# Kernel optimization log

Measured on AMD Instinct MI355X. Metric: run time of the kernel, lower is better.

Reference implementation:

```python
import jax, jax.numpy as jnp
import numpy as np

N = 8192        # nodes
E = 262144      # edges (avg degree 32)
D = 128         # input_dim
H = 128         # hidden_dim
O = 64          # output_dim (classes)
C = 4096        # codebook_size
LAMB_EDGE = 1.0
LAMB_NODE = 1.0
COMMIT_W = 0.25


def l2norm(x):
    return x / jnp.clip(jnp.linalg.norm(x, axis=-1, keepdims=True), 1e-12)


def graph_conv(x, W, b, src, dst, n):
    # DGL GraphConv, norm='both': D_out^{-1/2} on src, sum-aggregate, D_in^{-1/2} on dst, then xW+b, relu
    ones = jnp.ones(src.shape[0], x.dtype)
    deg_out = jax.ops.segment_sum(ones, src, num_segments=n)
    deg_in = jax.ops.segment_sum(ones, dst, num_segments=n)
    norm_src = jnp.where(deg_out > 0, jax.lax.rsqrt(jnp.maximum(deg_out, 1e-12)), 0.0)
    norm_dst = jnp.where(deg_in > 0, jax.lax.rsqrt(jnp.maximum(deg_in, 1e-12)), 0.0)
    h = x * norm_src[:, None]
    m = jax.ops.segment_sum(h[src], dst, num_segments=n)  # message passing (irregular gather/scatter)
    h = m * norm_dst[:, None]
    return jax.nn.relu(h @ W + b)


def setup_inputs() -> dict:
    key = jax.random.key(0)
    ks = jax.random.split(key, 16)
    feats = jax.random.normal(ks[0], (N, D), jnp.float32)
    src = jax.random.randint(ks[1], (E,), 0, N)
    dst = jax.random.randint(ks[2], (E,), 0, N)
    s = 1.0 / np.sqrt(D)
    sh = 1.0 / np.sqrt(H)
    return {
        'feats': feats, 'src': src, 'dst': dst,
        'W1': jax.random.normal(ks[3], (D, D), jnp.float32) * s,
        'b1': jnp.zeros((D,), jnp.float32),
        'W2': jax.random.normal(ks[4], (D, H), jnp.float32) * s,
        'b2': jnp.zeros((H,), jnp.float32),
        'dec1_W': jax.random.normal(ks[5], (D, D), jnp.float32) * s,
        'dec1_b': jnp.zeros((D,), jnp.float32),
        'dec2_W': jax.random.normal(ks[6], (D, D), jnp.float32) * s,
        'dec2_b': jnp.zeros((D,), jnp.float32),
        'lin_W': jax.random.normal(ks[7], (H, O), jnp.float32) * sh,
        'lin_b': jnp.zeros((O,), jnp.float32),
        'codebook': jax.random.normal(ks[8], (C, D), jnp.float32),
    }


def reference(feats, src, dst, W1, b1, W2, b2, dec1_W, dec1_b, dec2_W, dec2_b, lin_W, lin_b, codebook):
    n = feats.shape[0]
    # layer 1: GraphConv(D -> D)
    h1 = graph_conv(feats, W1, b1, src, dst, n)  # [N, D]

    # VectorQuantize with cosine similarity codebook
    xn = l2norm(h1)
    cn = l2norm(codebook)                 # [C, D]
    dist = xn @ cn.T                      # [N, C] cosine similarity
    ind = jnp.argmax(dist, axis=-1)       # [N]
    q = cn[ind]                           # [N, D] nearest (normalized) codes
    commit_loss = COMMIT_W * jnp.mean((jax.lax.stop_gradient(q) - h1) ** 2)
    quantized = h1 + jax.lax.stop_gradient(q - h1)  # straight-through

    quantized_edge = quantized @ dec1_W + dec1_b
    quantized_node = quantized @ dec2_W + dec2_b
    feature_rec_loss = LAMB_NODE * jnp.mean((h1 - quantized_node) ** 2)

    # dense adjacency reconstruction
    adj = jnp.zeros((n, n), feats.dtype).at[src, dst].set(1.0)
    adj_q = quantized_edge @ quantized_edge.T          # [N, N]
    adj_q = (adj_q - adj_q.min()) / (adj_q.max() - adj_q.min())
    edge_rec_loss = LAMB_EDGE * jnp.sqrt(jnp.mean((adj - adj_q) ** 2))

    # layer 2: GraphConv(D -> H) on quantized_edge, then linear head
    h3 = graph_conv(quantized_edge, W2, b2, src, dst, n)
    out = h3 @ lin_W + lin_b                           # [N, O]

    loss = feature_rec_loss + edge_rec_loss + commit_loss
    h_list = (h1, quantized, h3)
    return (h_list, out, loss, dist, cn)
```

## Files before the change

### kernel.cpp

```cpp
#include <hip/hip_runtime.h>
#include <cstdint>

constexpr int N = 8192, E = 262144, D = 128, O = 64, C = 4096;

#define DEV __device__ __forceinline__

typedef short s8v __attribute__((ext_vector_type(8)));
typedef float f4v __attribute__((ext_vector_type(4)));

DEV unsigned fmap(float f) {
  unsigned u = __float_as_uint(f);
  return (u & 0x80000000u) ? ~u : (u | 0x80000000u);
}
DEV unsigned short f2bf(float f) {
  uint32_t b = __float_as_uint(f);
  return (unsigned short)((b + 0x7FFFu + ((b >> 16) & 1u)) >> 16);
}


__global__ __launch_bounds__(256) void k_degree(const int* __restrict__ src, const int* __restrict__ dst,
    uint32_t* __restrict__ bits, int* __restrict__ dego, int* __restrict__ degi,
    uint32_t* __restrict__ scal_u) {
  int e = blockIdx.x * 256 + threadIdx.x;
  int s = src[e], d = dst[e];
  atomicAdd(&dego[s], 1);
  atomicAdd(&degi[d], 1);
  unsigned idx = (unsigned)s * 8192u + (unsigned)d;
  unsigned bit = 1u << (idx & 31);
  unsigned old = atomicOr(&bits[idx >> 5], bit);
  bool isnew = !(old & bit);
  unsigned long long b = __ballot(isnew);
  if ((threadIdx.x & 63) == 0) atomicAdd(&scal_u[2], (unsigned)__popcll(b));
}

__global__ __launch_bounds__(256) void k_norms(const int* __restrict__ dego, const int* __restrict__ degi,
                                               float* __restrict__ nsrc, float* __restrict__ ndst) {
  int i = blockIdx.x * 256 + threadIdx.x;
  if (i >= N) return;
  int a = dego[i], b = degi[i];
  nsrc[i] = a > 0 ? 1.0f / sqrtf((float)a) : 0.0f;
  ndst[i] = b > 0 ? 1.0f / sqrtf((float)b) : 0.0f;
}

__global__ __launch_bounds__(1024) void k_scan(const int* __restrict__ degi, int* __restrict__ rowptr,
                                               int* __restrict__ cursor) {
  __shared__ int sh[1024];
  int tid = threadIdx.x;
  int base = tid * 8;
  int v[8];
  int s = 0;
#pragma unroll
  for (int j = 0; j < 8; ++j) { v[j] = degi[base + j]; s += v[j]; }
  sh[tid] = s;
  __syncthreads();
  for (int off = 1; off < 1024; off <<= 1) {
    int t = (tid >= off) ? sh[tid - off] : 0;
    __syncthreads();
    sh[tid] += t;
    __syncthreads();
  }
  int run = (tid == 0) ? 0 : sh[tid - 1];
#pragma unroll
  for (int j = 0; j < 8; ++j) { rowptr[base + j] = run; cursor[base + j] = run; run += v[j]; }
  if (tid == 1023) rowptr[N] = run;
}

__global__ __launch_bounds__(256) void k_scatter(const int* __restrict__ src, const int* __restrict__ dst,
                                                 int* __restrict__ cursor, int* __restrict__ csr) {
  int e = blockIdx.x * 256 + threadIdx.x;
  int d = dst[e];
  int pos = atomicAdd(&cursor[d], 1);
  csr[pos] = src[e];
}

__global__ __launch_bounds__(256) void k_scale(const float4* __restrict__ in, const float* __restrict__ norm,
                                               float4* __restrict__ out) {
  int i = blockIdx.x * 256 + threadIdx.x;
  if (i >= N * 32) return;
  float s = norm[i >> 5];
  float4 v = in[i];
  v.x *= s; v.y *= s; v.z *= s; v.w *= s;
  out[i] = v;
}

__global__ __launch_bounds__(256) void k_tobf16(const float4* __restrict__ in, ushort4* __restrict__ out) {
  int i = blockIdx.x * 256 + threadIdx.x;
  if (i >= N * 32) return;
  float4 v = in[i];
  ushort4 o;
  o.x = f2bf(v.x); o.y = f2bf(v.y); o.z = f2bf(v.z); o.w = f2bf(v.w);
  out[i] = o;
}

__global__ __launch_bounds__(128) void k_aggregate(const int* __restrict__ rowptr, const int* __restrict__ csr,
    const float* __restrict__ tmp, const float* __restrict__ ndst, float* __restrict__ out) {
  int row = blockIdx.x, t = threadIdx.x;
  int e0 = rowptr[row], e1 = rowptr[row + 1];
  float acc = 0.f;
  int e = e0;
  for (; e + 4 <= e1; e += 4) {
    int s0 = csr[e], s1 = csr[e + 1], s2 = csr[e + 2], s3 = csr[e + 3];
    acc += tmp[s0 * 128 + t];
    acc += tmp[s1 * 128 + t];
    acc += tmp[s2 * 128 + t];
    acc += tmp[s3 * 128 + t];
  }
  for (; e < e1; ++e) acc += tmp[csr[e] * 128 + t];
  out[row * 128 + t] = acc * ndst[row];
}

__global__ __launch_bounds__(256) void k_l2norm(const float* __restrict__ in, float* __restrict__ out_al,
                                                float* __restrict__ out_extra, int rows) {
  int wave = threadIdx.x >> 6, lane = threadIdx.x & 63;
  int row = blockIdx.x * 4 + wave;
  if (row >= rows) return;
  float2 v = ((const float2*)in)[row * 64 + lane];
  float ss = v.x * v.x + v.y * v.y;
#pragma unroll
  for (int o = 32; o > 0; o >>= 1) ss += __shfl_xor(ss, o);
  float den = fmaxf(sqrtf(ss), 1e-12f);
  float ox = v.x / den, oy = v.y / den;
  ((float2*)out_al)[row * 64 + lane] = make_float2(ox, oy);
  if (out_extra != nullptr) {
    out_extra[row * 128 + 2 * lane] = ox;
    out_extra[row * 128 + 2 * lane + 1] = oy;
  }
}

template <int CO, bool RELU>
__global__ __launch_bounds__(256, 2) void k_mm(const float* __restrict__ A, const float* __restrict__ W,
    const float* __restrict__ bias, float* __restrict__ out) {
  constexpr int CG = CO / 4;
  constexpr int RG = 256 / CG;
  constexpr int TR = RG * 4;
  constexpr int WIT = (64 * CG) / 256;
  __shared__ __align__(16) float Al[TR * 128];
  __shared__ __align__(16) float Wl[64 * CO];
  int tid = threadIdx.x;
  int cg = tid % CG, rg = tid / CG;
  int rbase = blockIdx.x * TR;
#pragma unroll
  for (int it = 0; it < TR / 8; ++it) {
    int idx = tid + it * 256;
    int r = idx >> 5, c = idx & 31;
    *(float4*)&Al[r * 128 + c * 4] = *(const float4*)&A[(rbase + r) * 128 + c * 4];
  }
  float acc[4][4] = {};
  for (int kc = 0; kc < 128; kc += 64) {
    __syncthreads();
#pragma unroll
    for (int it = 0; it < WIT; ++it) {
      int idx = tid + it * 256;
      int r = idx / CG, c = idx % CG;
      *(float4*)&Wl[r * CO + c * 4] = *(const float4*)&W[(kc + r) * CO + c * 4];
    }
    __syncthreads();
#pragma unroll
    for (int k = 0; k < 64; ++k) {
      float4 w4 = *(const float4*)&Wl[k * CO + cg * 4];
#pragma unroll
      for (int i = 0; i < 4; ++i) {
        float a = Al[(rg * 4 + i) * 128 + kc + k];
        acc[i][0] += a * w4.x; acc[i][1] += a * w4.y; acc[i][2] += a * w4.z; acc[i][3] += a * w4.w;
      }
    }
  }
  float4 b4 = *(const float4*)&bias[cg * 4];
#pragma unroll
  for (int i = 0; i < 4; ++i) {
    float4 o;
    o.x = acc[i][0] + b4.x; o.y = acc[i][1] + b4.y; o.z = acc[i][2] + b4.z; o.w = acc[i][3] + b4.w;
    if (RELU) { o.x = fmaxf(o.x, 0.f); o.y = fmaxf(o.y, 0.f); o.z = fmaxf(o.z, 0.f); o.w = fmaxf(o.w, 0.f); }
    *(float4*)&out[(rbase + rg * 4 + i) * CO + cg * 4] = o;
  }
}

__global__ __launch_bounds__(256) void k_gemm(const float* __restrict__ A, const float* __restrict__ B,
    float* __restrict__ dout, unsigned long long* __restrict__ amax) {
  int bx = blockIdx.x, by = blockIdx.y;
  int rbase = by * 128, cbase = bx * 128;
  __shared__ __align__(16) float Al[128 * 36];
  __shared__ __align__(16) float Bl[128 * 36];
  int tid = threadIdx.x;
  int tx = tid & 15, ty = tid >> 4;
  float acc[8][8];
#pragma unroll
  for (int i = 0; i < 8; ++i)
#pragma unroll
    for (int j = 0; j < 8; ++j) acc[i][j] = 0.f;

  for (int kc = 0; kc < 128; kc += 32) {
#pragma unroll
    for (int it = 0; it < 4; ++it) {
      int idx = tid + it * 256;
      int r = idx >> 3, c = idx & 7;
      *(float4*)&Al[r * 36 + c * 4] = *(const float4*)&A[(rbase + r) * 128 + kc + c * 4];
      *(float4*)&Bl[r * 36 + c * 4] = *(const float4*)&B[(cbase + r) * 128 + kc + c * 4];
    }
    __syncthreads();
#pragma unroll 1
    for (int k4 = 0; k4 < 8; ++k4) {
      float4 a[8];
#pragma unroll
      for (int i = 0; i < 8; ++i) a[i] = *(const float4*)&Al[(ty + (i << 4)) * 36 + (k4 << 2)];
#pragma unroll
      for (int j = 0; j < 8; ++j) {
        float4 b = *(const float4*)&Bl[(tx + (j << 4)) * 36 + (k4 << 2)];
#pragma unroll
        for (int i = 0; i < 8; ++i)
          acc[i][j] += a[i].x * b.x + a[i].y * b.y + a[i].z * b.z + a[i].w * b.w;
      }
    }
    __syncthreads();
  }

  float bestv[8];
  int bestc[8];
#pragma unroll
  for (int i = 0; i < 8; ++i) { bestv[i] = -3.4e38f; bestc[i] = 0; }
#pragma unroll
  for (int i = 0; i < 8; ++i) {
    int row = rbase + ty + (i << 4);
#pragma unroll
    for (int j = 0; j < 8; ++j) {
      int col = cbase + tx + (j << 4);
      float v = acc[i][j];
      dout[row * 4096 + col] = v;
      if (v > bestv[i]) { bestv[i] = v; bestc[i] = col; }
    }
  }
  unsigned long long* sc = (unsigned long long*)Al;
#pragma unroll
  for (int i = 0; i < 8; ++i)
    sc[(ty + (i << 4)) * 16 + tx] =
        (((unsigned long long)fmap(bestv[i])) << 32) | (unsigned long long)(0xFFFFFFFFu - (unsigned)bestc[i]);
  __syncthreads();
  if (tid < 128) {
    unsigned long long m = 0ull;
#pragma unroll
    for (int k = 0; k < 16; ++k) {
      unsigned long long t = sc[tid * 16 + k];
      m = t > m ? t : m;
    }
    atomicMax(&amax[rbase + tid], m);
  }
}

__global__ __launch_bounds__(256) void k_adjq(const unsigned short* __restrict__ qb,
    const uint32_t* __restrict__ bits,
    double* __restrict__ p_sum, double* __restrict__ p_sq, double* __restrict__ p_es,
    float* __restrict__ p_mn, float* __restrict__ p_mx) {
  int bx = blockIdx.x, by = blockIdx.y;
  int pid = by * gridDim.x + bx;
  int tid = threadIdx.x;
  if (bx < by) {
    if (tid == 0) {
      p_sum[pid] = 0.0; p_sq[pid] = 0.0; p_es[pid] = 0.0;
      p_mn[pid] = 3.4e38f; p_mx[pid] = -3.4e38f;
    }
    return;
  }
  int rbase = by * 128, cbase = bx * 128;
  __shared__ unsigned short Ab[128 * 132];
  __shared__ unsigned short Bb[128 * 132];
#pragma unroll
  for (int it = 0; it < 8; ++it) {
    int idx = tid + it * 256;
    int r = idx >> 4, ch = idx & 15;
    *(s8v*)&Ab[r * 132 + ch * 8] = *(const s8v*)&qb[(rbase + r) * 128 + ch * 8];
    *(s8v*)&Bb[r * 132 + ch * 8] = *(const s8v*)&qb[(cbase + r) * 128 + ch * 8];
  }
  __syncthreads();
  int wave = tid >> 6, lane = tid & 63;
  int l15 = lane & 15, quad = lane >> 4;
  int wr = wave * 32;
  f4v acc[2][8];
#pragma unroll
  for (int rt = 0; rt < 2; ++rt)
#pragma unroll
    for (int ct = 0; ct < 8; ++ct) acc[rt][ct] = {0.f, 0.f, 0.f, 0.f};
  s8v a[2][4];
#pragma unroll
  for (int rt = 0; rt < 2; ++rt)
#pragma unroll
    for (int kq = 0; kq < 4; ++kq)
      a[rt][kq] = *(const s8v*)&Ab[(wr + rt * 16 + l15) * 132 + kq * 32 + quad * 8];
#pragma unroll
  for (int ct = 0; ct < 8; ++ct) {
    s8v b[4];
#pragma unroll
    for (int kq = 0; kq < 4; ++kq)
      b[kq] = *(const s8v*)&Bb[(ct * 16 + l15) * 132 + kq * 32 + quad * 8];
#pragma unroll
    for (int rt = 0; rt < 2; ++rt)
#pragma unroll
      for (int kq = 0; kq < 4; ++kq)
        acc[rt][ct] = __builtin_amdgcn_mfma_f32_16x16x32_bf16(a[rt][kq], b[kq], acc[rt][ct], 0, 0, 0);
  }
  __syncthreads();
  uint32_t* bl = (uint32_t*)Ab;
  uint32_t* blT = bl + 512;
#pragma unroll
  for (int it = 0; it < 2; ++it) {
    int idx = tid + it * 256;
    int r = idx >> 2, wq = idx & 3;
    bl[idx] = bits[(rbase + r) * 256 + (cbase >> 5) + wq];
    blT[idx] = bits[(cbase + r) * 256 + (rbase >> 5) + wq];
  }
  __syncthreads();
  float lsum = 0.f, lsq = 0.f, les = 0.f;
  float lmin = 3.4e38f, lmax = -3.4e38f;
  bool diag = (bx == by);
#pragma unroll
  for (int rt = 0; rt < 2; ++rt)
#pragma unroll
    for (int ct = 0; ct < 8; ++ct)
#pragma unroll
      for (int reg = 0; reg < 4; ++reg) {
        int lr = wr + rt * 16 + quad * 4 + reg;
        int lc = ct * 16 + l15;
        if (diag && lc < lr) continue;
        float v = acc[rt][ct][reg];
        bool ondiag = diag && (lc == lr);
        float wgt = ondiag ? 1.f : 2.f;
        lsum += wgt * v;
        lsq += wgt * v * v;
        lmin = fminf(lmin, v);
        lmax = fmaxf(lmax, v);
        unsigned eb = (bl[lr * 4 + (lc >> 5)] >> (lc & 31)) & 1u;
        if (!ondiag) eb += (blT[lc * 4 + (lr >> 5)] >> (lr & 31)) & 1u;
        if (eb) les += (float)eb * v;
      }
  double dsum = (double)lsum, dsq = (double)lsq, des = (double)les;
#pragma unroll
  for (int o = 32; o > 0; o >>= 1) {
    dsum += __shfl_xor(dsum, o);
    dsq += __shfl_xor(dsq, o);
    des += __shfl_xor(des, o);
    lmin = fminf(lmin, __shfl_xor(lmin, o));
    lmax = fmaxf(lmax, __shfl_xor(lmax, o));
  }
  double* shd = (double*)Bb;
  float* shf = (float*)(shd + 12);
  if (lane == 0) {
    shd[wave * 3 + 0] = dsum; shd[wave * 3 + 1] = dsq; shd[wave * 3 + 2] = des;
    shf[wave * 2 + 0] = lmin; shf[wave * 2 + 1] = lmax;
  }
  __syncthreads();
  if (tid == 0) {
    double s = 0.0, q = 0.0, e = 0.0;
    float m0 = 3.4e38f, m1 = -3.4e38f;
#pragma unroll
    for (int w0 = 0; w0 < 4; ++w0) {
      s += shd[w0 * 3 + 0]; q += shd[w0 * 3 + 1]; e += shd[w0 * 3 + 2];
      m0 = fminf(m0, shf[w0 * 2 + 0]); m1 = fmaxf(m1, shf[w0 * 2 + 1]);
    }
    p_sum[pid] = s; p_sq[pid] = q; p_es[pid] = e;
    p_mn[pid] = m0; p_mx[pid] = m1;
  }
}

__global__ __launch_bounds__(128) void k_q(const unsigned long long* __restrict__ amax,
    const float* __restrict__ cnws, const float* __restrict__ h1, float* __restrict__ qout,
    float* __restrict__ pq) {
  int row = blockIdx.x, t = threadIdx.x;
  unsigned long long key = amax[row];
  int col = (int)(0xFFFFFFFFu - (uint32_t)(key & 0xFFFFFFFFull));
  float q = cnws[col * 128 + t];
  qout[row * 128 + t] = q;
  float dd = q - h1[row * 128 + t];
  float ss = dd * dd;
#pragma unroll
  for (int o = 32; o > 0; o >>= 1) ss += __shfl_xor(ss, o);
  __shared__ float p[2];
  if ((t & 63) == 0) p[t >> 6] = ss;
  __syncthreads();
  if (t == 0) pq[row] = p[0] + p[1];
}

__global__ __launch_bounds__(256) void k_sqdiff(const float4* __restrict__ a, const float4* __restrict__ b,
                                                float* __restrict__ ps) {
  int i = blockIdx.x * 256 + threadIdx.x;
  float s = 0.f;
  const int total = N * 32;
  for (; i < total; i += gridDim.x * 256) {
    float4 x = a[i], y = b[i];
    float d0 = x.x - y.x, d1 = x.y - y.y, d2 = x.z - y.z, d3 = x.w - y.w;
    s += d0 * d0 + d1 * d1 + d2 * d2 + d3 * d3;
  }
#pragma unroll
  for (int o = 32; o > 0; o >>= 1) s += __shfl_xor(s, o);
  __shared__ float p[4];
  if ((threadIdx.x & 63) == 0) p[threadIdx.x >> 6] = s;
  __syncthreads();
  if (threadIdx.x == 0) ps[blockIdx.x] = p[0] + p[1] + p[2] + p[3];
}

__global__ __launch_bounds__(1024) void k_finish(const double* __restrict__ p_sum,
    const double* __restrict__ p_sq, const double* __restrict__ p_es,
    const float* __restrict__ p_mn, const float* __restrict__ p_mx,
    const float* __restrict__ pq, const float* __restrict__ ps,
    const uint32_t* __restrict__ scal_u, float* __restrict__ o_loss) {
  int tid = threadIdx.x;
  double sum = 0.0, sq = 0.0, es = 0.0, commit = 0.0, frec = 0.0;
  float mn = 3.4e38f, mx = -3.4e38f;
  for (int i = tid; i < 4096; i += 1024) {
    sum += p_sum[i]; sq += p_sq[i]; es += p_es[i];
    mn = fminf(mn, p_mn[i]); mx = fmaxf(mx, p_mx[i]);
  }
  for (int i = tid; i < 8192; i += 1024) commit += (double)pq[i];
  if (tid < 512) frec = (double)ps[tid];
#pragma unroll
  for (int o = 32; o > 0; o >>= 1) {
    sum += __shfl_xor(sum, o); sq += __shfl_xor(sq, o); es += __shfl_xor(es, o);
    commit += __shfl_xor(commit, o); frec += __shfl_xor(frec, o);
    mn = fminf(mn, __shfl_xor(mn, o)); mx = fmaxf(mx, __shfl_xor(mx, o));
  }
  __shared__ double shd[16][5];
  __shared__ float shf[16][2];
  int wave = tid >> 6, lane = tid & 63;
  if (lane == 0) {
    shd[wave][0] = sum; shd[wave][1] = sq; shd[wave][2] = es;
    shd[wave][3] = commit; shd[wave][4] = frec;
    shf[wave][0] = mn; shf[wave][1] = mx;
  }
  __syncthreads();
  if (tid == 0) {
    double s = 0, q = 0, e = 0, c = 0, f = 0;
    float m0 = 3.4e38f, m1 = -3.4e38f;
    for (int w0 = 0; w0 < 16; ++w0) {
      s += shd[w0][0]; q += shd[w0][1]; e += shd[w0][2]; c += shd[w0][3]; f += shd[w0][4];
      m0 = fminf(m0, shf[w0][0]); m1 = fmaxf(m1, shf[w0][1]);
    }
    double mnd = (double)m0, mxd = (double)m1, U = (double)scal_u[2];
    const double N2 = 67108864.0;
    double scl = 1.0 / (mxd - mnd);
    double mean = (scl * scl * (q - 2.0 * mnd * s + mnd * mnd * N2) - 2.0 * scl * (e - mnd * U) + U) / N2;
    *o_loss = (float)(f / 1048576.0 + sqrt(mean) + 0.25 * c / 1048576.0);
  }
}

extern "C" void kernel_launch(void* const* d_in, const int* in_sizes, int n_in,
                              void* d_out, int out_size, void* d_ws, size_t ws_size,
                              hipStream_t stream) {
  (void)in_sizes; (void)n_in; (void)out_size;
  const float* feats = (const float*)d_in[0];
  const int* src = (const int*)d_in[1];
  const int* dst = (const int*)d_in[2];
  const float* W1 = (const float*)d_in[3];
  const float* b1 = (const float*)d_in[4];
  const float* W2 = (const float*)d_in[5];
  const float* b2 = (const float*)d_in[6];
  const float* dec1W = (const float*)d_in[7];
  const float* dec1b = (const float*)d_in[8];
  const float* dec2W = (const float*)d_in[9];
  const float* dec2b = (const float*)d_in[10];
  const float* linW = (const float*)d_in[11];
  const float* linb = (const float*)d_in[12];
  const float* codebook = (const float*)d_in[13];

  float* out = (float*)d_out;
  float* o_h1 = out;
  float* o_q = out + 1048576;
  float* o_h3 = out + 2097152;
  float* o_out = out + 3145728;
  float* o_loss = out + 3670016;
  float* o_dist = out + 3670017;
  float* o_cn = out + 37224449;

  char* w = (char*)d_ws;
  size_t off = 0;
  auto alloc = [&](size_t b) { char* p = w + off; off = (off + b + 255) & ~(size_t)255; return p; };
  uint32_t* bits = (uint32_t*)alloc(8388608);
  int* dego = (int*)alloc(N * 4);
  int* degi = (int*)alloc(N * 4);
  unsigned long long* amax = (unsigned long long*)alloc(N * 8);
  uint32_t* scal_u = (uint32_t*)alloc(256);
  size_t zero_bytes = off;
  int* rowptr = (int*)alloc((N + 1) * 4);
  int* cursor = (int*)alloc(N * 4);
  int* csr = (int*)alloc(E * 4);
  float* nsrc = (float*)alloc(N * 4);
  float* ndst = (float*)alloc(N * 4);
  float* tmp = (float*)alloc((size_t)N * D * 4);
  float* agg = (float*)alloc((size_t)N * D * 4);
  float* xn = (float*)alloc((size_t)N * D * 4);
  float* cnws = (float*)alloc((size_t)C * D * 4);
  float* qe = (float*)alloc((size_t)N * D * 4);
  float* qn = (float*)alloc((size_t)N * D * 4);
  double* p_sum = (double*)alloc(4096 * 8);
  double* p_sq = (double*)alloc(4096 * 8);
  double* p_es = (double*)alloc(4096 * 8);
  float* p_mn = (float*)alloc(4096 * 4);
  float* p_mx = (float*)alloc(4096 * 4);
  float* pq = (float*)alloc(8192 * 4);
  float* ps = (float*)alloc(512 * 4);
  unsigned short* qb = (unsigned short*)tmp;
  if (ws_size < off) return;

  hipMemsetAsync(d_ws, 0, zero_bytes, stream);

  k_degree<<<E / 256, 256, 0, stream>>>(src, dst, bits, dego, degi, scal_u);
  k_norms<<<N / 256, 256, 0, stream>>>(dego, degi, nsrc, ndst);
  k_scan<<<1, 1024, 0, stream>>>(degi, rowptr, cursor);
  k_scatter<<<E / 256, 256, 0, stream>>>(src, dst, cursor, csr);

  k_scale<<<N * 32 / 256, 256, 0, stream>>>((const float4*)feats, nsrc, (float4*)tmp);
  k_aggregate<<<N, 128, 0, stream>>>(rowptr, csr, tmp, ndst, agg);
  k_mm<128, true><<<N / 32, 256, 0, stream>>>(agg, W1, b1, o_h1);

  k_l2norm<<<C / 4, 256, 0, stream>>>(codebook, cnws, o_cn, C);
  k_l2norm<<<N / 4, 256, 0, stream>>>(o_h1, xn, nullptr, N);
  k_gemm<<<dim3(C / 128, N / 128), 256, 0, stream>>>(xn, cnws, o_dist, amax);
  k_q<<<N, 128, 0, stream>>>(amax, cnws, o_h1, o_q, pq);

  k_mm<128, false><<<N / 32, 256, 0, stream>>>(o_q, dec1W, dec1b, qe);
  k_mm<128, false><<<N / 32, 256, 0, stream>>>(o_q, dec2W, dec2b, qn);
  k_sqdiff<<<512, 256, 0, stream>>>((const float4*)o_h1, (const float4*)qn, ps);

  k_tobf16<<<N * 32 / 256, 256, 0, stream>>>((const float4*)qe, (ushort4*)qb);
  k_adjq<<<dim3(N / 128, N / 128), 256, 0, stream>>>(qb, bits, p_sum, p_sq, p_es, p_mn, p_mx);

  k_scale<<<N * 32 / 256, 256, 0, stream>>>((const float4*)qe, nsrc, (float4*)tmp);
  k_aggregate<<<N, 128, 0, stream>>>(rowptr, csr, tmp, ndst, agg);
  k_mm<128, true><<<N / 32, 256, 0, stream>>>(agg, W2, b2, o_h3);
  k_mm<64, false><<<N / 64, 256, 0, stream>>>(o_h3, linW, linb, o_out);

  k_finish<<<1, 1024, 0, stream>>>(p_sum, p_sq, p_es, p_mn, p_mx, pq, ps, scal_u, o_loss);
}
```

Measured before the change: 544.1 us.

## Compute cosine-similarity GEMM with split-bf16 MFMA and exact fp32 argmax fallback

Replaces the fp32 FMA-based N×C cosine-similarity GEMM with an MFMA kernel that splits each operand into bf16 hi and lo parts and sums three products (hi·hi, lo·hi, hi·lo) to approximate fp32 accuracy. Each tile also records its top-2 values, and the quantize kernel reduces these per row. When the top-2 gap is below a threshold, it recomputes the argmax exactly in fp32 to keep index selection robust. The goal is to move the dominant 8192×4096×128 GEMM onto matrix cores, at the cost of two split kernels, extra partial buffers, and possible precision drift in the stored dist output.

After: 606.4 us. +11.5%, slower.

```diff
diff --git a/kernel.cpp b/kernel.cpp
--- a/kernel.cpp
+++ b/kernel.cpp
@@ -12,10 +12,15 @@
   unsigned u = __float_as_uint(f);
   return (u & 0x80000000u) ? ~u : (u | 0x80000000u);
 }
+DEV float funmap(unsigned u) {
+  unsigned o = (u & 0x80000000u) ? (u & 0x7FFFFFFFu) : ~u;
+  return __uint_as_float(o);
+}
 DEV unsigned short f2bf(float f) {
   uint32_t b = __float_as_uint(f);
   return (unsigned short)((b + 0x7FFFu + ((b >> 16) & 1u)) >> 16);
 }
+DEV float bf2f(unsigned short h) { return __uint_as_float((uint32_t)h << 16); }
 
 
 __global__ __launch_bounds__(256) void k_degree(const int* __restrict__ src, const int* __restrict__ dst,
@@ -92,6 +97,18 @@
   out[i] = o;
 }
 
+__global__ __launch_bounds__(256) void k_split(const float4* __restrict__ in,
+    ushort4* __restrict__ hi, ushort4* __restrict__ lo, int n4) {
+  int i = blockIdx.x * 256 + threadIdx.x;
+  if (i >= n4) return;
+  float4 v = in[i];
+  ushort4 h, l;
+  h.x = f2bf(v.x); h.y = f2bf(v.y); h.z = f2bf(v.z); h.w = f2bf(v.w);
+  l.x = f2bf(v.x - bf2f(h.x)); l.y = f2bf(v.y - bf2f(h.y));
+  l.z = f2bf(v.z - bf2f(h.z)); l.w = f2bf(v.w - bf2f(h.w));
+  hi[i] = h; lo[i] = l;
+}
+
 __global__ __launch_bounds__(128) void k_aggregate(const int* __restrict__ rowptr, const int* __restrict__ csr,
     const float* __restrict__ tmp, const float* __restrict__ ndst, float* __restrict__ out) {
   int row = blockIdx.x, t = threadIdx.x;
@@ -175,75 +192,196 @@
   }
 }
 
-__global__ __launch_bounds__(256) void k_gemm(const float* __restrict__ A, const float* __restrict__ B,
-    float* __restrict__ dout, unsigned long long* __restrict__ amax) {
+__global__ __launch_bounds__(256) void k_dist(
+    const unsigned short* __restrict__ xhi, const unsigned short* __restrict__ xlo,
+    const unsigned short* __restrict__ chi, const unsigned short* __restrict__ clo,
+    float* __restrict__ dout, unsigned long long* __restrict__ pbk, float* __restrict__ pbv2) {
   int bx = blockIdx.x, by = blockIdx.y;
   int rbase = by * 128, cbase = bx * 128;
-  __shared__ __align__(16) float Al[128 * 36];
-  __shared__ __align__(16) float Bl[128 * 36];
+  __shared__ __align__(16) unsigned short As[128 * 132];
+  __shared__ __align__(16) unsigned short Bs[128 * 132];
   int tid = threadIdx.x;
-  int tx = tid & 15, ty = tid >> 4;
-  float acc[8][8];
-#pragma unroll
-  for (int i = 0; i < 8; ++i)
-#pragma unroll
-    for (int j = 0; j < 8; ++j) acc[i][j] = 0.f;
-
-  for (int kc = 0; kc < 128; kc += 32) {
-#pragma unroll
-    for (int it = 0; it < 4; ++it) {
-      int idx = tid + it * 256;
-      int r = idx >> 3, c = idx & 7;
-      *(float4*)&Al[r * 36 + c * 4] = *(const float4*)&A[(rbase + r) * 128 + kc + c * 4];
-      *(float4*)&Bl[r * 36 + c * 4] = *(const float4*)&B[(cbase + r) * 128 + kc + c * 4];
-    }
-    __syncthreads();
-#pragma unroll 1
-    for (int k4 = 0; k4 < 8; ++k4) {
-      float4 a[8];
-#pragma unroll
-      for (int i = 0; i < 8; ++i) a[i] = *(const float4*)&Al[(ty + (i << 4)) * 36 + (k4 << 2)];
-#pragma unroll
-      for (int j = 0; j < 8; ++j) {
-        float4 b = *(const float4*)&Bl[(tx + (j << 4)) * 36 + (k4 << 2)];
-#pragma unroll
-        for (int i = 0; i < 8; ++i)
-          acc[i][j] += a[i].x * b.x + a[i].y * b.y + a[i].z * b.z + a[i].w * b.w;
+  int wave = tid >> 6, lane = tid & 63;
+  int l15 = lane & 15, quad = lane >> 4;
+  int wr = wave * 32;
+
+#pragma unroll
+  for (int it = 0; it < 8; ++it) {
+    int idx = tid + it * 256;
+    int r = idx >> 4, ch = idx & 15;
+    *(s8v*)&As[r * 132 + ch * 8] = *(const s8v*)&xhi[(rbase + r) * 128 + ch * 8];
+    *(s8v*)&Bs[r * 132 + ch * 8] = *(const s8v*)&chi[(cbase + r) * 128 + ch * 8];
+  }
+  __syncthreads();
+  s8v ah[2][4], al[2][4];
+#pragma unroll
+  for (int rt = 0; rt < 2; ++rt)
+#pragma unroll
+    for (int kq = 0; kq < 4; ++kq)
+      ah[rt][kq] = *(const s8v*)&As[(wr + rt * 16 + l15) * 132 + kq * 32 + quad * 8];
+  __syncthreads();
+#pragma unroll
+  for (int it = 0; it < 8; ++it) {
+    int idx = tid + it * 256;
+    int r = idx >> 4, ch = idx & 15;
+    *(s8v*)&As[r * 132 + ch * 8] = *(const s8v*)&xlo[(rbase + r) * 128 + ch * 8];
+  }
+  __syncthreads();
+#pragma unroll
+  for (int rt = 0; rt < 2; ++rt)
+#pragma unroll
+    for (int kq = 0; kq < 4; ++kq)
+      al[rt][kq] = *(const s8v*)&As[(wr + rt * 16 + l15) * 132 + kq * 32 + quad * 8];
+
+  f4v acc[2][8];
+#pragma unroll
+  for (int rt = 0; rt < 2; ++rt)
+#pragma unroll
+    for (int ct = 0; ct < 8; ++ct) acc[rt][ct] = {0.f, 0.f, 0.f, 0.f};
+
+#pragma unroll
+  for (int ct = 0; ct < 8; ++ct) {
+    s8v b[4];
+#pragma unroll
+    for (int kq = 0; kq < 4; ++kq)
+      b[kq] = *(const s8v*)&Bs[(ct * 16 + l15) * 132 + kq * 32 + quad * 8];
+#pragma unroll
+    for (int rt = 0; rt < 2; ++rt)
+#pragma unroll
+      for (int kq = 0; kq < 4; ++kq) {
+        acc[rt][ct] = __builtin_amdgcn_mfma_f32_16x16x32_bf16(ah[rt][kq], b[kq], acc[rt][ct], 0, 0, 0);
+        acc[rt][ct] = __builtin_amdgcn_mfma_f32_16x16x32_bf16(al[rt][kq], b[kq], acc[rt][ct], 0, 0, 0);
       }
-    }
-    __syncthreads();
-  }
-
-  float bestv[8];
-  int bestc[8];
-#pragma unroll
-  for (int i = 0; i < 8; ++i) { bestv[i] = -3.4e38f; bestc[i] = 0; }
-#pragma unroll
-  for (int i = 0; i < 8; ++i) {
-    int row = rbase + ty + (i << 4);
-#pragma unroll
-    for (int j = 0; j < 8; ++j) {
-      int col = cbase + tx + (j << 4);
-      float v = acc[i][j];
-      dout[row * 4096 + col] = v;
-      if (v > bestv[i]) { bestv[i] = v; bestc[i] = col; }
-    }
-  }
-  unsigned long long* sc = (unsigned long long*)Al;
-#pragma unroll
-  for (int i = 0; i < 8; ++i)
-    sc[(ty + (i << 4)) * 16 + tx] =
-        (((unsigned long long)fmap(bestv[i])) << 32) | (unsigned long long)(0xFFFFFFFFu - (unsigned)bestc[i]);
+  }
+  __syncthreads();
+#pragma unroll
+  for (int it = 0; it < 8; ++it) {
+    int idx = tid + it * 256;
+    int r = idx >> 4, ch = idx & 15;
+    *(s8v*)&Bs[r * 132 + ch * 8] = *(const s8v*)&clo[(cbase + r) * 128 + ch * 8];
+  }
+  __syncthreads();
+#pragma unroll
+  for (int ct = 0; ct < 8; ++ct) {
+    s8v b[4];
+#pragma unroll
+    for (int kq = 0; kq < 4; ++kq)
+      b[kq] = *(const s8v*)&Bs[(ct * 16 + l15) * 132 + kq * 32 + quad * 8];
+#pragma unroll
+    for (int rt = 0; rt < 2; ++rt)
+#pragma unroll
+      for (int kq = 0; kq < 4; ++kq)
+        acc[rt][ct] = __builtin_amdgcn_mfma_f32_16x16x32_bf16(ah[rt][kq], b[kq], acc[rt][ct], 0, 0, 0);
+  }
+
+  float b1v[2][4], b2v[2][4];
+  unsigned c1v[2][4];
+#pragma unroll
+  for (int rt = 0; rt < 2; ++rt)
+#pragma unroll
+    for (int reg = 0; reg < 4; ++reg) { b1v[rt][reg] = -3.4e38f; b2v[rt][reg] = -3.4e38f; c1v[rt][reg] = 0; }
+#pragma unroll
+  for (int rt = 0; rt < 2; ++rt)
+#pragma unroll
+    for (int ct = 0; ct < 8; ++ct)
+#pragma unroll
+      for (int reg = 0; reg < 4; ++reg) {
+        float v = acc[rt][ct][reg];
+        int row = rbase + wr + rt * 16 + quad * 4 + reg;
+        int col = cbase + ct * 16 + l15;
+        dout[(size_t)row * 4096 + col] = v;
+        if (v > b1v[rt][reg]) { b2v[rt][reg] = b1v[rt][reg]; b1v[rt][reg] = v; c1v[rt][reg] = (unsigned)col; }
+        else if (v > b2v[rt][reg]) b2v[rt][reg] = v;
+      }
+  __syncthreads();
+  unsigned long long* sck = (unsigned long long*)As;
+  float* scv = (float*)Bs;
+#pragma unroll
+  for (int rt = 0; rt < 2; ++rt)
+#pragma unroll
+    for (int reg = 0; reg < 4; ++reg) {
+      int rloc = wr + rt * 16 + quad * 4 + reg;
+      sck[rloc * 16 + l15] =
+          (((unsigned long long)fmap(b1v[rt][reg])) << 32) |
+          (unsigned long long)(0xFFFFFFFFu - c1v[rt][reg]);
+      scv[rloc * 16 + l15] = b2v[rt][reg];
+    }
   __syncthreads();
   if (tid < 128) {
     unsigned long long m = 0ull;
 #pragma unroll
-    for (int k = 0; k < 16; ++k) {
-      unsigned long long t = sc[tid * 16 + k];
+    for (int l = 0; l < 16; ++l) {
+      unsigned long long t = sck[tid * 16 + l];
       m = t > m ? t : m;
     }
-    atomicMax(&amax[rbase + tid], m);
-  }
+    float v2 = -3.4e38f;
+#pragma unroll
+    for (int l = 0; l < 16; ++l) {
+      unsigned long long k = sck[tid * 16 + l];
+      float c = (k == m) ? scv[tid * 16 + l] : funmap((unsigned)(k >> 32));
+      v2 = fmaxf(v2, c);
+    }
+    pbk[(size_t)(rbase + tid) * 32 + bx] = m;
+    pbv2[(size_t)(rbase + tid) * 32 + bx] = v2;
+  }
+}
+
+__global__ __launch_bounds__(128) void k_q(const unsigned long long* __restrict__ pbk,
+    const float* __restrict__ pbv2, const float* __restrict__ xn, const float* __restrict__ cnws,
+    const float* __restrict__ h1, float* __restrict__ qout, float* __restrict__ pq) {
+  int row = blockIdx.x, t = threadIdx.x;
+  int e = t & 31;
+  unsigned long long k = pbk[(size_t)row * 32 + e];
+  float v2l = pbv2[(size_t)row * 32 + e];
+  unsigned long long m = k;
+#pragma unroll
+  for (int o = 32; o > 0; o >>= 1) {
+    unsigned long long s = __shfl_xor(m, o);
+    m = s > m ? s : m;
+  }
+  float cand = (k == m) ? v2l : funmap((unsigned)(k >> 32));
+#pragma unroll
+  for (int o = 32; o > 0; o >>= 1) cand = fmaxf(cand, __shfl_xor(cand, o));
+  float gap = funmap((unsigned)(m >> 32)) - cand;
+  int col;
+  __shared__ float xr[128];
+  __shared__ unsigned long long bw[2];
+  if (gap < 2e-4f) {
+    xr[t] = xn[row * 128 + t];
+    __syncthreads();
+    unsigned long long best = 0ull;
+    for (int i = 0; i < 32; ++i) {
+      int c = t + i * 128;
+      const float* cp = &cnws[c * 128];
+      float s = 0.f;
+#pragma unroll 8
+      for (int kk = 0; kk < 128; ++kk) s += xr[kk] * cp[kk];
+      unsigned long long key = (((unsigned long long)fmap(s)) << 32) |
+                               (unsigned long long)(0xFFFFFFFFu - (unsigned)c);
+      if (key > best) best = key;
+    }
+#pragma unroll
+    for (int o = 32; o > 0; o >>= 1) {
+      unsigned long long s2 = __shfl_xor(best, o);
+      best = s2 > best ? s2 : best;
+    }
+    if ((t & 63) == 0) bw[t >> 6] = best;
+    __syncthreads();
+    best = bw[0] > bw[1] ? bw[0] : bw[1];
+    col = (int)(0xFFFFFFFFu - (unsigned)(best & 0xFFFFFFFFull));
+  } else {
+    col = (int)(0xFFFFFFFFu - (unsigned)(m & 0xFFFFFFFFull));
+  }
+  float q = cnws[col * 128 + t];
+  qout[row * 128 + t] = q;
+  float dd = q - h1[row * 128 + t];
+  float ss = dd * dd;
+#pragma unroll
+  for (int o = 32; o > 0; o >>= 1) ss += __shfl_xor(ss, o);
+  __shared__ float p[2];
+  if ((t & 63) == 0) p[t >> 6] = ss;
+  __syncthreads();
+  if (t == 0) pq[row] = p[0] + p[1];
 }
 
 __global__ __launch_bounds__(256) void k_adjq(const unsigned short* __restrict__ qb,
@@ -358,24 +496,6 @@
     p_sum[pid] = s; p_sq[pid] = q; p_es[pid] = e;
     p_mn[pid] = m0; p_mx[pid] = m1;
   }
-}
-
-__global__ __launch_bounds__(128) void k_q(const unsigned long long* __restrict__ amax,
-    const float* __restrict__ cnws, const float* __restrict__ h1, float* __restrict__ qout,
-    float* __restrict__ pq) {
-  int row = blockIdx.x, t = threadIdx.x;
-  unsigned long long key = amax[row];
-  int col = (int)(0xFFFFFFFFu - (uint32_t)(key & 0xFFFFFFFFull));
-  float q = cnws[col * 128 + t];
-  qout[row * 128 + t] = q;
-  float dd = q - h1[row * 128 + t];
-  float ss = dd * dd;
-#pragma unroll
-  for (int o = 32; o > 0; o >>= 1) ss += __shfl_xor(ss, o);
-  __shared__ float p[2];
-  if ((t & 63) == 0) p[t >> 6] = ss;
-  __syncthreads();
-  if (t == 0) pq[row] = p[0] + p[1];
 }
 
 __global__ __launch_bounds__(256) void k_sqdiff(const float4* __restrict__ a, const float4* __restrict__ b,
@@ -474,7 +594,6 @@
   uint32_t* bits = (uint32_t*)alloc(8388608);
   int* dego = (int*)alloc(N * 4);
   int* degi = (int*)alloc(N * 4);
-  unsigned long long* amax = (unsigned long long*)alloc(N * 8);
   uint32_t* scal_u = (uint32_t*)alloc(256);
   size_t zero_bytes = off;
   int* rowptr = (int*)alloc((N + 1) * 4);
@@ -496,6 +615,12 @@
   float* pq = (float*)alloc(8192 * 4);
   float* ps = (float*)alloc(512 * 4);
   unsigned short* qb = (unsigned short*)tmp;
+  unsigned short* xhi = (unsigned short*)qe;
+  unsigned short* xlo = (unsigned short*)(qe + 524288);
+  unsigned short* chi = (unsigned short*)qn;
+  unsigned short* clo = (unsigned short*)(qn + 262144);
+  unsigned long long* pbk = (unsigned long long*)agg;
+  float* pbv2 = (float*)(agg + 524288);
   if (ws_size < off) return;
 
   hipMemsetAsync(d_ws, 0, zero_bytes, stream);
@@ -511,8 +636,10 @@
 
   k_l2norm<<<C / 4, 256, 0, stream>>>(codebook, cnws, o_cn, C);
   k_l2norm<<<N / 4, 256, 0, stream>>>(o_h1, xn, nullptr, N);
-  k_gemm<<<dim3(C / 128, N / 128), 256, 0, stream>>>(xn, cnws, o_dist, amax);
-  k_q<<<N, 128, 0, stream>>>(amax, cnws, o_h1, o_q, pq);
+  k_split<<<N * 32 / 256, 256, 0, stream>>>((const float4*)xn, (ushort4*)xhi, (ushort4*)xlo, N * 32);
+  k_split<<<C * 32 / 256, 256, 0, stream>>>((const float4*)cnws, (ushort4*)chi, (ushort4*)clo, C * 32);
+  k_dist<<<dim3(C / 128, N / 128), 256, 0, stream>>>(xhi, xlo, chi, clo, o_dist, pbk, pbv2);
+  k_q<<<N, 128, 0, stream>>>(pbk, pbv2, xn, cnws, o_h1, o_q, pq);
 
   k_mm<128, false><<<N / 32, 256, 0, stream>>>(o_q, dec1W, dec1b, qe);
   k_mm<128, false><<<N / 32, 256, 0, stream>>>(o_q, dec2W, dec2b, qn);
```
